# Kernel tuning notes

Hardware: AMD Instinct MI355X
Metric: run time of the kernel (lower is better)

The kernel has to match this reference:

```python
import jax, jax.numpy as jnp
import numpy as np

B, S, HID = 1, 4096, 2048
H, KVH, D = 8, 4, 256
SW = 1024          # sliding window
EPS = 1e-6
NEG = -1e30


def _rmsnorm(x, w=None, eps=EPS):
    # torch nn.RMSNorm: x / sqrt(mean(x^2) + eps) * weight
    y = x * jax.lax.rsqrt(jnp.mean(x * x, axis=-1, keepdims=True) + eps)
    return y * w if w is not None else y


def _rotate_half(x):
    x1, x2 = jnp.split(x, 2, axis=-1)
    return jnp.concatenate([-x2, x1], axis=-1)


def _rope(x, cos, sin):
    # x: [B,S,H,D]; cos/sin: [B,S,rot] -> [B,S,1,rot]; rot == D here (no pass-through)
    c = cos[:, :, None, :]
    s = sin[:, :, None, :]
    return x * c + _rotate_half(x) * s


def setup_inputs() -> dict:
    key = jax.random.key(0)
    ks = jax.random.split(key, 9)
    return {
        "hidden_states": jax.random.normal(ks[0], (B, S, HID), jnp.float32),
        "cos": jax.random.uniform(ks[1], (B, S, D), jnp.float32),
        "sin": jax.random.uniform(ks[2], (B, S, D), jnp.float32),
        "q_w": jax.random.normal(ks[3], (H * D, HID), jnp.float32) * 0.02,
        "k_w": jax.random.normal(ks[4], (KVH * D, HID), jnp.float32) * 0.02,
        "v_w": jax.random.normal(ks[5], (KVH * D, HID), jnp.float32) * 0.02,
        "o_w": jax.random.normal(ks[6], (HID, H * D), jnp.float32) * 0.02,
        "q_norm_w": jnp.ones((D,), jnp.float32),
        "k_norm_w": jnp.ones((D,), jnp.float32),
    }


def reference(hidden_states, cos, sin, q_w, k_w, v_w, o_w, q_norm_w, k_norm_w):
    b, s, _ = hidden_states.shape
    # Projections (no bias), reshape to [B,S,heads,D]
    q = (hidden_states @ q_w.T).reshape(b, s, H, D)
    k = (hidden_states @ k_w.T).reshape(b, s, KVH, D)
    v = (hidden_states @ v_w.T).reshape(b, s, KVH, D)
    # per-head RMSNorm (v_norm has no affine), then RoPE on q/k
    q = _rope(_rmsnorm(q, q_norm_w), cos, sin)
    k = _rope(_rmsnorm(k, k_norm_w), cos, sin)
    v = _rmsnorm(v)
    # flatten(0,1): packed tokens T = B*S
    T = b * s
    q = q.reshape(T, H, D).transpose(1, 0, 2)          # [H,T,D]
    k = k.reshape(T, KVH, D).transpose(1, 0, 2)        # [KVH,T,D]
    v = v.reshape(T, KVH, D).transpose(1, 0, 2)
    # GQA: repeat_interleave kv heads
    rep = H // KVH
    k = jnp.repeat(k, rep, axis=0)                     # [H,T,D]
    v = jnp.repeat(v, rep, axis=0)
    # causal + sliding-window mask (allowed: i-SW < j <= i), scale=1.0
    i = jnp.arange(T)[:, None]
    j = jnp.arange(T)[None, :]
    allowed = (j <= i) & ((i - j) < SW)                # [T,T] bool
    scores = jnp.einsum("htd,hsd->hts", q, k)          # [H,T,T]
    scores = jnp.where(allowed[None], scores, NEG)
    p = jax.nn.softmax(scores, axis=-1)
    out = jnp.einsum("hts,hsd->htd", p, v)             # [H,T,D]
    out = out.transpose(1, 0, 2).reshape(b, s, H * D)
    return out @ o_w.T
```

## Files before the change

### kernel.cpp

```cpp
#include <hip/hip_runtime.h>
#include <stdint.h>

typedef __bf16 bf16x8 __attribute__((ext_vector_type(8)));
typedef __bf16 bf16x4 __attribute__((ext_vector_type(4)));
typedef float f32x4v __attribute__((ext_vector_type(4)));

__device__ __forceinline__ void async_copy16(const void* gptr, void* ldsptr) {
  __builtin_amdgcn_global_load_lds(
      (const __attribute__((address_space(1))) void*)gptr,
      (__attribute__((address_space(3))) void*)ldsptr,
      16, 0, 0);
}

__global__ __launch_bounds__(256) void cvt_split(
    const float* __restrict__ src, __bf16* __restrict__ hi,
    __bf16* __restrict__ lo, int n4) {
  const int i = blockIdx.x * 256 + threadIdx.x;
  if (i < n4) {
    const float4 v = ((const float4*)src)[i];
    float vv[4] = {v.x, v.y, v.z, v.w};
    bf16x4 h, l;
    for (int j = 0; j < 4; ++j) {
      h[j] = (__bf16)vv[j];
      l[j] = (__bf16)(vv[j] - (float)h[j]);
    }
    ((bf16x4*)hi)[i] = h;
    ((bf16x4*)lo)[i] = l;
  }
}

__global__ __launch_bounds__(256, 2) void gemm_qkv(
    const __bf16* __restrict__ Ah, const __bf16* __restrict__ Al,
    const __bf16* __restrict__ Bh, const __bf16* __restrict__ Bl,
    float* __restrict__ C) {
  const int K = 2048, ldc = 4096;
  __shared__ __align__(16) __bf16 Ash[128 * 32];
  __shared__ __align__(16) __bf16 Asl[128 * 32];
  __shared__ __align__(16) __bf16 Bsh[128 * 32];
  __shared__ __align__(16) __bf16 Bsl[128 * 32];
  const int m0 = blockIdx.y * 128, n0 = blockIdx.x * 128;
  const int tid = threadIdx.x;
  const int wid = tid >> 6, lane = tid & 63, l15 = lane & 15, quad = lane >> 4;
  const int wm = wid >> 1, wn = wid & 1;

  f32x4v acc[4][4] = {};

  for (int kb = 0; kb < K; kb += 32) {
    for (int it = 0; it < 2; ++it) {
      const int c = (wid * 2 + it) * 64 + lane;
      const int row = c >> 2, col = (c & 3) * 8;
      const size_t ao = (size_t)(m0 + row) * K + kb + col;
      const size_t bo = (size_t)(n0 + row) * K + kb + col;
      const int dst = (wid * 2 + it) * 512;
      async_copy16(Ah + ao, &Ash[dst]);
      async_copy16(Al + ao, &Asl[dst]);
      async_copy16(Bh + bo, &Bsh[dst]);
      async_copy16(Bl + bo, &Bsl[dst]);
    }
    __syncthreads();
    bf16x8 afh[4], afl[4], bfh[4], bfl[4];
    for (int mt = 0; mt < 4; ++mt) {
      const int o = (wm * 64 + mt * 16 + l15) * 32 + quad * 8;
      afh[mt] = *(const bf16x8*)&Ash[o];
      afl[mt] = *(const bf16x8*)&Asl[o];
    }
    for (int nt = 0; nt < 4; ++nt) {
      const int o = (wn * 64 + nt * 16 + l15) * 32 + quad * 8;
      bfh[nt] = *(const bf16x8*)&Bsh[o];
      bfl[nt] = *(const bf16x8*)&Bsl[o];
    }
    for (int mt = 0; mt < 4; ++mt)
      for (int nt = 0; nt < 4; ++nt) {
        acc[mt][nt] = __builtin_amdgcn_mfma_f32_16x16x32_bf16(afh[mt], bfh[nt], acc[mt][nt], 0, 0, 0);
        acc[mt][nt] = __builtin_amdgcn_mfma_f32_16x16x32_bf16(afh[mt], bfl[nt], acc[mt][nt], 0, 0, 0);
        acc[mt][nt] = __builtin_amdgcn_mfma_f32_16x16x32_bf16(afl[mt], bfh[nt], acc[mt][nt], 0, 0, 0);
      }
    __syncthreads();
  }
  for (int mt = 0; mt < 4; ++mt)
    for (int nt = 0; nt < 4; ++nt) {
      const int row = m0 + wm * 64 + mt * 16 + quad * 4;
      const int col = n0 + wn * 64 + nt * 16 + l15;
      for (int r = 0; r < 4; ++r)
        C[(size_t)(row + r) * ldc + col] = acc[mt][nt][r];
    }
}

__global__ __launch_bounds__(64) void norm_rope(
    const float* __restrict__ qkv, const float* __restrict__ cosb,
    const float* __restrict__ sinb, const float* __restrict__ qnw,
    const float* __restrict__ knw,
    __bf16* __restrict__ qh, __bf16* __restrict__ ql,
    __bf16* __restrict__ kh, __bf16* __restrict__ kl,
    __bf16* __restrict__ vT) {
  const int s = blockIdx.x, c = blockIdx.y, lane = threadIdx.x;
  const int d0 = lane * 4;
  const float4 xv = *(const float4*)(qkv + (size_t)s * 4096 + c * 256 + d0);
  float v[4] = {xv.x, xv.y, xv.z, xv.w};
  float ss = v[0] * v[0] + v[1] * v[1] + v[2] * v[2] + v[3] * v[3];
  for (int off = 1; off < 64; off <<= 1) ss += __shfl_xor(ss, off);
  const float rn = rsqrtf(ss * (1.0f / 256.0f) + 1e-6f);
  if (c < 12) {
    const float* w = (c < 8) ? qnw : knw;
    float y[4], yp[4];
    for (int j = 0; j < 4; ++j) y[j] = v[j] * rn * w[d0 + j];
    for (int j = 0; j < 4; ++j) yp[j] = __shfl_xor(y[j], 32);
    for (int j = 0; j < 4; ++j) {
      const int d = d0 + j;
      const float rot = (d < 128) ? -yp[j] : yp[j];
      y[j] = y[j] * cosb[s * 256 + d] + rot * sinb[s * 256 + d];
    }
    const size_t o = (c < 8) ? ((size_t)c * 4096 + s) * 256 + d0
                             : ((size_t)(c - 8) * 4096 + s) * 256 + d0;
    __bf16* dh = (c < 8) ? qh : kh;
    __bf16* dl = (c < 8) ? ql : kl;
    bf16x4 hv, lv;
    for (int j = 0; j < 4; ++j) {
      hv[j] = (__bf16)y[j];
      lv[j] = (__bf16)(y[j] - (float)hv[j]);
    }
    *(bf16x4*)(dh + o) = hv;
    *(bf16x4*)(dl + o) = lv;
  } else {
    const int kvh = c - 12;
    for (int j = 0; j < 4; ++j)
      vT[(size_t)(kvh * 256 + d0 + j) * 4096 + s] = (__bf16)(v[j] * rn);
  }
}

__global__ __launch_bounds__(512, 2) void attn_mfma(
    const __bf16* __restrict__ Qh_, const __bf16* __restrict__ Ql_,
    const __bf16* __restrict__ Kh_, const __bf16* __restrict__ Kl_,
    const __bf16* __restrict__ VT, __bf16* __restrict__ Aout) {
  const int S = 4096, D = 256;
  const int bid = blockIdx.y * 32 + blockIdx.x;
  const int swz = (bid & 7) * 32 + (bid >> 3);
  const int h = swz >> 5;
  const int q0 = (swz & 31) * 128;
  const int tid = threadIdx.x;
  const int wid = tid >> 6, lane = tid & 63, l15 = lane & 15, quad = lane >> 4;
  const int kv = h >> 1;

  __shared__ __align__(16) __bf16 Ksh[2][32 * 256];
  __shared__ __align__(16) __bf16 Ksl[2][32 * 256];
  __shared__ __align__(16) __bf16 Vs[2][256 * 32];
  __shared__ __align__(16) __bf16 P[8][16][32];

  const __bf16* Khh = Kh_ + (size_t)kv * S * D;
  const __bf16* Khl = Kl_ + (size_t)kv * S * D;
  const __bf16* Vh = VT + (size_t)kv * D * S;

  auto stage = [&](int buf, int kt) {
    for (int set = 0; set < 2; ++set) {
      const int n = set * 512 + wid * 64 + lane;
      const int row = n >> 5, c = n & 31;
      const int sc = c ^ (row & 7);
      const size_t go = (size_t)(kt + row) * D + sc * 8;
      const int dst = (set * 512 + wid * 64) * 8;
      async_copy16(Khh + go, &Ksh[buf][dst]);
      async_copy16(Khl + go, &Ksl[buf][dst]);
      const int dim = n >> 2, kc = n & 3;
      const size_t vo = (size_t)dim * S + kt + kc * 8;
      async_copy16(Vh + vo, &Vs[buf][dst]);
    }
  };

  bf16x8 qfh[8], qfl[8];
  {
    const size_t qoff =
        (size_t)h * S * D + (size_t)(q0 + wid * 16 + l15) * D + quad * 8;
    for (int ks = 0; ks < 8; ++ks) {
      qfh[ks] = *(const bf16x8*)(Qh_ + qoff + ks * 32);
      qfl[ks] = *(const bf16x8*)(Ql_ + qoff + ks * 32);
    }
  }

  f32x4v O[16] = {};
  float mrow[4] = {-1e30f, -1e30f, -1e30f, -1e30f};
  float lrow[4] = {0.f, 0.f, 0.f, 0.f};

  const int lo = (q0 >= 1024) ? (q0 - 1024) : 0;
  const int hi = q0 + 96;
  const int iqmin = q0 + wid * 16;
  const int iqmax = iqmin + 15;

  stage(0, lo);
  __syncthreads();
  int cur = 0;

  for (int kt = lo; kt <= hi; kt += 32) {
    if (kt + 32 <= hi) stage(cur ^ 1, kt + 32);
    const bool active = (kt <= iqmax) && (kt + 31 >= iqmin - 1023);
    if (active) {
      f32x4v sa[2] = {};
      for (int nt = 0; nt < 2; ++nt) {
        const int row = nt * 16 + l15;
        const int rx = row & 7;
        for (int ks = 0; ks < 8; ++ks) {
          const int c = (ks * 4 + quad) ^ rx;
          const bf16x8 kh8 = *(const bf16x8*)&Ksh[cur][row * 256 + c * 8];
          const bf16x8 kl8 = *(const bf16x8*)&Ksl[cur][row * 256 + c * 8];
          sa[nt] = __builtin_amdgcn_mfma_f32_16x16x32_bf16(qfh[ks], kh8, sa[nt], 0, 0, 0);
          sa[nt] = __builtin_amdgcn_mfma_f32_16x16x32_bf16(qfh[ks], kl8, sa[nt], 0, 0, 0);
          sa[nt] = __builtin_amdgcn_mfma_f32_16x16x32_bf16(qfl[ks], kh8, sa[nt], 0, 0, 0);
        }
      }
      float al[4];
      for (int r = 0; r < 4; ++r) {
        const int i = q0 + wid * 16 + quad * 4 + r;
        float mx = -1e30f;
        for (int nt = 0; nt < 2; ++nt) {
          const int j = kt + nt * 16 + l15;
          const float svv = ((j <= i) && (i - j < 1024)) ? sa[nt][r] : -1e30f;
          sa[nt][r] = svv;
          mx = fmaxf(mx, svv);
        }
        for (int off = 1; off < 16; off <<= 1) mx = fmaxf(mx, __shfl_xor(mx, off));
        const float mn = fmaxf(mrow[r], mx);
        al[r] = __expf(mrow[r] - mn);
        float ps = 0.f;
        for (int nt = 0; nt < 2; ++nt) {
          const float p = (mn <= -1e29f) ? 0.f : __expf(sa[nt][r] - mn);
          P[wid][quad * 4 + r][nt * 16 + l15] = (__bf16)p;
          ps += p;
        }
        for (int off = 1; off < 16; off <<= 1) ps += __shfl_xor(ps, off);
        lrow[r] = lrow[r] * al[r] + ps;
        mrow[r] = mn;
      }
      for (int nt2 = 0; nt2 < 16; ++nt2)
        for (int r = 0; r < 4; ++r) O[nt2][r] *= al[r];
      __asm__ volatile("s_waitcnt lgkmcnt(0)" ::: "memory");
      __builtin_amdgcn_sched_barrier(0);
      const bf16x8 pf = *(const bf16x8*)&P[wid][l15][quad * 8];
      for (int nt2 = 0; nt2 < 16; ++nt2) {
        const int dim = nt2 * 16 + l15;
        const bf16x8 vf = *(const bf16x8*)&Vs[cur][(dim * 4 + quad) * 8];
        O[nt2] = __builtin_amdgcn_mfma_f32_16x16x32_bf16(pf, vf, O[nt2], 0, 0, 0);
      }
    }
    __syncthreads();
    cur ^= 1;
  }
  for (int nt2 = 0; nt2 < 16; ++nt2)
    for (int r = 0; r < 4; ++r) {
      const float o = O[nt2][r] / lrow[r];
      Aout[(size_t)(q0 + wid * 16 + quad * 4 + r) * 2048 + h * 256 + nt2 * 16 + l15] = (__bf16)o;
    }
}

__global__ __launch_bounds__(256, 2) void gemm_out(
    const __bf16* __restrict__ A, const float* __restrict__ B,
    float* __restrict__ C) {
  const int K = 2048, ldc = 2048;
  __shared__ __align__(16) __bf16 As[128 * 32];
  __shared__ __align__(16) __bf16 Bs[128 * 32];
  const int m0 = blockIdx.y * 128, n0 = blockIdx.x * 128;
  const int tid = threadIdx.x;
  const int wid = tid >> 6, lane = tid & 63, l15 = lane & 15, quad = lane >> 4;
  const int wm = wid >> 1, wn = wid & 1;

  f32x4v acc[4][4] = {};

  for (int kb = 0; kb < K; kb += 32) {
    for (int cc = 0; cc < 2; ++cc) {
      const int c = cc * 256 + tid;
      const int row = c >> 2, col = (c & 3) * 8;
      *(bf16x8*)&As[row * 32 + col] =
          *(const bf16x8*)(A + (size_t)(m0 + row) * K + kb + col);
    }
    for (int cc = 0; cc < 4; ++cc) {
      const int c = cc * 256 + tid;
      const int row = c >> 3, col = (c & 7) * 4;
      const float4 bv = *(const float4*)(B + (size_t)(n0 + row) * K + kb + col);
      bf16x4 bh = {(__bf16)bv.x, (__bf16)bv.y, (__bf16)bv.z, (__bf16)bv.w};
      *(bf16x4*)&Bs[row * 32 + col] = bh;
    }
    __syncthreads();
    bf16x8 af[4], bfr[4];
    for (int mt = 0; mt < 4; ++mt)
      af[mt] = *(const bf16x8*)&As[(wm * 64 + mt * 16 + l15) * 32 + quad * 8];
    for (int nt = 0; nt < 4; ++nt)
      bfr[nt] = *(const bf16x8*)&Bs[(wn * 64 + nt * 16 + l15) * 32 + quad * 8];
    for (int mt = 0; mt < 4; ++mt)
      for (int nt = 0; nt < 4; ++nt)
        acc[mt][nt] = __builtin_amdgcn_mfma_f32_16x16x32_bf16(af[mt], bfr[nt], acc[mt][nt], 0, 0, 0);
    __syncthreads();
  }
  for (int mt = 0; mt < 4; ++mt)
    for (int nt = 0; nt < 4; ++nt) {
      const int row = m0 + wm * 64 + mt * 16 + quad * 4;
      const int col = n0 + wn * 64 + nt * 16 + l15;
      for (int r = 0; r < 4; ++r)
        C[(size_t)(row + r) * ldc + col] = acc[mt][nt][r];
    }
}

extern "C" void kernel_launch(void* const* d_in, const int* in_sizes, int n_in,
                              void* d_out, int out_size, void* d_ws, size_t ws_size,
                              hipStream_t stream) {
  const float* hidden = (const float*)d_in[0];
  const float* cosb   = (const float*)d_in[1];
  const float* sinb   = (const float*)d_in[2];
  const float* qw     = (const float*)d_in[3];
  const float* kw     = (const float*)d_in[4];
  const float* vw     = (const float*)d_in[5];
  const float* ow     = (const float*)d_in[6];
  const float* qnw    = (const float*)d_in[7];
  const float* knw    = (const float*)d_in[8];
  float* out = (float*)d_out;

  const size_t MB = 1048576;
  char* ws = (char*)d_ws;
  float*  qkvf = (float*)ws;
  __bf16* attn = (__bf16*)ws;
  __bf16* hh   = (__bf16*)(ws + 64 * MB);
  __bf16* hl   = (__bf16*)(ws + 80 * MB);
  __bf16* wh   = (__bf16*)(ws + 96 * MB);
  __bf16* wl   = (__bf16*)(ws + 112 * MB);
  __bf16* qh   = (__bf16*)(ws + 64 * MB);
  __bf16* ql   = (__bf16*)(ws + 80 * MB);
  __bf16* kh   = (__bf16*)(ws + 96 * MB);
  __bf16* kl   = (__bf16*)(ws + 104 * MB);
  __bf16* vT   = (__bf16*)(ws + 112 * MB);

  cvt_split<<<dim3(8192), 256, 0, stream>>>(hidden, hh, hl, 2097152);
  cvt_split<<<dim3(4096), 256, 0, stream>>>(qw, wh, wl, 1048576);
  cvt_split<<<dim3(2048), 256, 0, stream>>>(kw, wh + 4194304, wl + 4194304, 524288);
  cvt_split<<<dim3(2048), 256, 0, stream>>>(vw, wh + 6291456, wl + 6291456, 524288);

  gemm_qkv<<<dim3(32, 32), 256, 0, stream>>>(hh, hl, wh, wl, qkvf);
  norm_rope<<<dim3(4096, 16), 64, 0, stream>>>(qkvf, cosb, sinb, qnw, knw,
                                               qh, ql, kh, kl, vT);
  attn_mfma<<<dim3(32, 8), 512, 0, stream>>>(qh, ql, kh, kl, vT, attn);
  gemm_out<<<dim3(16, 32), 256, 0, stream>>>(attn, ow, out);
}
```

Measured before the change: 586.8 us.

## Restructure QKV GEMM with double-buffered LDS, 8 waves, swizzle and block remap

The QKV split-bf16 GEMM moves to 512 threads (8 waves in a 2x4 grid), a K-tile of 64 and double-buffered LDS, so the next tile loads asynchronously while MFMAs run on the current one. LDS rows are XOR-swizzled to avoid bank conflicts. Block IDs are remapped for L2 locality, and MFMA issue is interleaved with A-fragment reloads using barriers and setprio. LDS use grows to 128KB per block, which limits occupancy to one block per CU.

```diff
diff --git a/kernel.cpp b/kernel.cpp
--- a/kernel.cpp
+++ b/kernel.cpp
@@ -29,58 +29,106 @@
   }
 }
 
-__global__ __launch_bounds__(256, 2) void gemm_qkv(
+__global__ __launch_bounds__(512, 2) void gemm_qkv(
     const __bf16* __restrict__ Ah, const __bf16* __restrict__ Al,
     const __bf16* __restrict__ Bh, const __bf16* __restrict__ Bl,
     float* __restrict__ C) {
   const int K = 2048, ldc = 4096;
-  __shared__ __align__(16) __bf16 Ash[128 * 32];
-  __shared__ __align__(16) __bf16 Asl[128 * 32];
-  __shared__ __align__(16) __bf16 Bsh[128 * 32];
-  __shared__ __align__(16) __bf16 Bsl[128 * 32];
-  const int m0 = blockIdx.y * 128, n0 = blockIdx.x * 128;
+  __shared__ __align__(16) __bf16 Ash[2][128 * 64];
+  __shared__ __align__(16) __bf16 Asl[2][128 * 64];
+  __shared__ __align__(16) __bf16 Bsh[2][128 * 64];
+  __shared__ __align__(16) __bf16 Bsl[2][128 * 64];
+
+  const int bid0 = blockIdx.y * 32 + blockIdx.x;
+  const int bid = (bid0 & 7) * 128 + (bid0 >> 3);
+  const int m0 = (bid >> 5) * 128, n0 = (bid & 31) * 128;
+
   const int tid = threadIdx.x;
   const int wid = tid >> 6, lane = tid & 63, l15 = lane & 15, quad = lane >> 4;
-  const int wm = wid >> 1, wn = wid & 1;
-
-  f32x4v acc[4][4] = {};
-
-  for (int kb = 0; kb < K; kb += 32) {
-    for (int it = 0; it < 2; ++it) {
-      const int c = (wid * 2 + it) * 64 + lane;
-      const int row = c >> 2, col = (c & 3) * 8;
-      const size_t ao = (size_t)(m0 + row) * K + kb + col;
-      const size_t bo = (size_t)(n0 + row) * K + kb + col;
-      const int dst = (wid * 2 + it) * 512;
-      async_copy16(Ah + ao, &Ash[dst]);
-      async_copy16(Al + ao, &Asl[dst]);
-      async_copy16(Bh + bo, &Bsh[dst]);
-      async_copy16(Bl + bo, &Bsl[dst]);
-    }
+  const int wm = wid >> 2, wn = wid & 3;
+  const int rx = l15 & 7;
+
+  f32x4v acc[4][2] = {};
+
+  auto stage = [&](int buf, int kb) {
+    for (int set = 0; set < 2; ++set) {
+      const int p = set * 512 + wid * 64 + lane;
+      const int row = p >> 3;
+      const int sc = (p & 7) ^ (row & 7);
+      const size_t ao = (size_t)(m0 + row) * K + kb + sc * 8;
+      const size_t bo = (size_t)(n0 + row) * K + kb + sc * 8;
+      const int dst = (set * 512 + wid * 64) * 8;
+      async_copy16(Ah + ao, &Ash[buf][dst]);
+      async_copy16(Al + ao, &Asl[buf][dst]);
+      async_copy16(Bh + bo, &Bsh[buf][dst]);
+      async_copy16(Bl + bo, &Bsl[buf][dst]);
+    }
+  };
+
+  stage(0, 0);
+  __syncthreads();
+
+  for (int t = 0; t < 32; ++t) {
+    const int buf = t & 1;
+    bf16x8 bh[2][2], bl2[2][2];
+#pragma unroll
+    for (int nt = 0; nt < 2; ++nt) {
+      const int r = wn * 32 + nt * 16 + l15;
+#pragma unroll
+      for (int ks = 0; ks < 2; ++ks) {
+        const int o = r * 64 + (((ks * 4 + quad) ^ rx) * 8);
+        bh[nt][ks] = *(const bf16x8*)&Bsh[buf][o];
+        bl2[nt][ks] = *(const bf16x8*)&Bsl[buf][o];
+      }
+    }
+    bf16x8 ah[2], al2[2];
+    {
+      const int r = wm * 64 + 0 * 16 + l15;
+#pragma unroll
+      for (int ks = 0; ks < 2; ++ks) {
+        const int o = r * 64 + (((ks * 4 + quad) ^ rx) * 8);
+        ah[ks] = *(const bf16x8*)&Ash[buf][o];
+        al2[ks] = *(const bf16x8*)&Asl[buf][o];
+      }
+    }
+    if (t < 31) stage(buf ^ 1, (t + 1) * 64);
+
+#pragma unroll
+    for (int mt = 0; mt < 4; ++mt) {
+      __builtin_amdgcn_s_barrier();
+      __asm__ volatile("s_waitcnt lgkmcnt(0)" ::: "memory");
+      __builtin_amdgcn_sched_barrier(0);
+      __builtin_amdgcn_s_setprio(1);
+#pragma unroll
+      for (int nt = 0; nt < 2; ++nt)
+#pragma unroll
+        for (int ks = 0; ks < 2; ++ks) {
+          acc[mt][nt] = __builtin_amdgcn_mfma_f32_16x16x32_bf16(ah[ks], bh[nt][ks], acc[mt][nt], 0, 0, 0);
+          acc[mt][nt] = __builtin_amdgcn_mfma_f32_16x16x32_bf16(ah[ks], bl2[nt][ks], acc[mt][nt], 0, 0, 0);
+          acc[mt][nt] = __builtin_amdgcn_mfma_f32_16x16x32_bf16(al2[ks], bh[nt][ks], acc[mt][nt], 0, 0, 0);
+        }
+      __builtin_amdgcn_s_setprio(0);
+      if (mt < 3) {
+        const int r = wm * 64 + (mt + 1) * 16 + l15;
+#pragma unroll
+        for (int ks = 0; ks < 2; ++ks) {
+          const int o = r * 64 + (((ks * 4 + quad) ^ rx) * 8);
+          ah[ks] = *(const bf16x8*)&Ash[buf][o];
+          al2[ks] = *(const bf16x8*)&Asl[buf][o];
+        }
+      }
+    }
+    __builtin_amdgcn_sched_barrier(0);
     __syncthreads();
-    bf16x8 afh[4], afl[4], bfh[4], bfl[4];
-    for (int mt = 0; mt < 4; ++mt) {
-      const int o = (wm * 64 + mt * 16 + l15) * 32 + quad * 8;
-      afh[mt] = *(const bf16x8*)&Ash[o];
-      afl[mt] = *(const bf16x8*)&Asl[o];
-    }
-    for (int nt = 0; nt < 4; ++nt) {
-      const int o = (wn * 64 + nt * 16 + l15) * 32 + quad * 8;
-      bfh[nt] = *(const bf16x8*)&Bsh[o];
-      bfl[nt] = *(const bf16x8*)&Bsl[o];
-    }
-    for (int mt = 0; mt < 4; ++mt)
-      for (int nt = 0; nt < 4; ++nt) {
-        acc[mt][nt] = __builtin_amdgcn_mfma_f32_16x16x32_bf16(afh[mt], bfh[nt], acc[mt][nt], 0, 0, 0);
-        acc[mt][nt] = __builtin_amdgcn_mfma_f32_16x16x32_bf16(afh[mt], bfl[nt], acc[mt][nt], 0, 0, 0);
-        acc[mt][nt] = __builtin_amdgcn_mfma_f32_16x16x32_bf16(afl[mt], bfh[nt], acc[mt][nt], 0, 0, 0);
-      }
-    __syncthreads();
-  }
+  }
+
+#pragma unroll
   for (int mt = 0; mt < 4; ++mt)
-    for (int nt = 0; nt < 4; ++nt) {
+#pragma unroll
+    for (int nt = 0; nt < 2; ++nt) {
       const int row = m0 + wm * 64 + mt * 16 + quad * 4;
-      const int col = n0 + wn * 64 + nt * 16 + l15;
+      const int col = n0 + wn * 32 + nt * 16 + l15;
+#pragma unroll
       for (int r = 0; r < 4; ++r)
         C[(size_t)(row + r) * ldc + col] = acc[mt][nt][r];
     }
@@ -195,9 +243,9 @@
       f32x4v sa[2] = {};
       for (int nt = 0; nt < 2; ++nt) {
         const int row = nt * 16 + l15;
-        const int rx = row & 7;
+        const int rxk = row & 7;
         for (int ks = 0; ks < 8; ++ks) {
-          const int c = (ks * 4 + quad) ^ rx;
+          const int c = (ks * 4 + quad) ^ rxk;
           const bf16x8 kh8 = *(const bf16x8*)&Ksh[cur][row * 256 + c * 8];
           const bf16x8 kl8 = *(const bf16x8*)&Ksl[cur][row * 256 + c * 8];
           sa[nt] = __builtin_amdgcn_mfma_f32_16x16x32_bf16(qfh[ks], kh8, sa[nt], 0, 0, 0);
@@ -329,7 +377,7 @@
   cvt_split<<<dim3(2048), 256, 0, stream>>>(kw, wh + 4194304, wl + 4194304, 524288);
   cvt_split<<<dim3(2048), 256, 0, stream>>>(vw, wh + 6291456, wl + 6291456, 524288);
 
-  gemm_qkv<<<dim3(32, 32), 256, 0, stream>>>(hh, hl, wh, wl, qkvf);
+  gemm_qkv<<<dim3(32, 32), 512, 0, stream>>>(hh, hl, wh, wl, qkvf);
   norm_rope<<<dim3(4096, 16), 64, 0, stream>>>(qkvf, cosb, sinb, qnw, knw,
                                                qh, ql, kh, kl, vT);
   attn_mfma<<<dim3(32, 8), 512, 0, stream>>>(qh, ql, kh, kl, vT, attn);
```

Result: slower. 600.9 us (+2.4%).
